# Kernel tuning notes

Hardware: AMD Instinct MI355X
Metric: run time of the kernel (lower is better)

## Reference

```python
import jax, jax.numpy as jnp
import numpy as np

B, S, D = 4, 2048, 1024
H, ADIM = 16, 64
HID = H * ADIM  # 1024


def setup_inputs() -> dict:
    key = jax.random.key(0)
    k1, k2, k3, k4 = jax.random.split(key, 4)
    iQ = jax.random.normal(k1, (B, S, D), dtype=jnp.float32)
    mask = jax.random.randint(k2, (B, S, S), 0, 2).astype(bool)
    Wa = jax.random.normal(k3, (3 * HID, D), dtype=jnp.float32) * (1.0 / np.sqrt(D))
    Wo = jax.random.normal(k4, (HID, HID), dtype=jnp.float32) * (1.0 / np.sqrt(HID))
    return {"iQ": iQ, "mask": mask, "Wa": Wa, "Wo": Wo}


def reference(iQ, mask, Wa, Wo):
    b, s, _ = iQ.shape
    # fused QKV projection: [B,S,3*HID]
    qkv = jnp.einsum("bsd,ed->bse", iQ, Wa)
    q, k, v = jnp.split(qkv, 3, axis=-1)
    # [B,S,HID] -> [B,H,S,ADIM]
    to_heads = lambda t: t.reshape(b, s, H, ADIM).transpose(0, 2, 1, 3)
    q, k, v = to_heads(q), to_heads(k), to_heads(v)
    scores = jnp.einsum("bhqd,bhkd->bhqk", q, k) / np.sqrt(ADIM).astype(np.float32)
    scores = jnp.where(mask[:, None, :, :], jnp.float32(-1e32), scores)
    attn = jax.nn.softmax(scores, axis=-1)
    o = jnp.einsum("bhqk,bhkd->bhqd", attn, v)
    o = o.transpose(0, 2, 1, 3).reshape(b, s, HID)
    return jnp.einsum("bse,oe->bso", o, Wo)
```

## Files before the change

kernel.cpp:

```cpp
#include <hip/hip_runtime.h>
#include <hip/hip_bf16.h>

typedef __bf16 bf16;
typedef __bf16 bfrag __attribute__((ext_vector_type(8)));
typedef float f32x4 __attribute__((ext_vector_type(4)));

constexpr int Bc = 4, Sc = 2048, Hc = 16, ADc = 64, HIDc = 1024;
constexpr size_t QKV_ELEMS = (size_t)Bc * Hc * Sc * ADc;

__device__ __forceinline__ void gload_lds16(const void* g, void* lds) {
  __builtin_amdgcn_global_load_lds(
      (const __attribute__((address_space(1))) unsigned int*)g,
      (__attribute__((address_space(3))) unsigned int*)lds, 16, 0, 0);
}

__device__ __forceinline__ bfrag ldb(const bf16* p) {
  return *(const bfrag*)p;
}

__global__ __launch_bounds__(256) void f2b(const float* __restrict__ s,
                                           bf16* __restrict__ d) {
  const size_t i = ((size_t)blockIdx.x * 256 + threadIdx.x) * 8;
  const float4 a = *(const float4*)(s + i);
  const float4 b = *(const float4*)(s + i + 4);
  bfrag o = {(bf16)a.x, (bf16)a.y, (bf16)a.z, (bf16)a.w,
             (bf16)b.x, (bf16)b.y, (bf16)b.z, (bf16)b.w};
  *(bfrag*)(d + i) = o;
}

template <int MODE>
__global__ __launch_bounds__(256) void gemm_bt(
    const bf16* __restrict__ A,
    const bf16* __restrict__ Bm,
    bf16* __restrict__ C0,
    bf16* __restrict__ C1,
    bf16* __restrict__ C2,
    float* __restrict__ Cf,
    int Kdim, int Ndim)
{
  __shared__ __align__(16) bf16 As[128 * 32];
  __shared__ __align__(16) bf16 Bs[128 * 32];

  const int tid  = threadIdx.x;
  const int wave = tid >> 6;
  const int lane = tid & 63;
  const int n16  = lane & 15;
  const int quad = lane >> 4;
  const int wm   = wave & 1;
  const int wn   = wave >> 1;
  const int m0   = blockIdx.y * 128;
  const int n0   = blockIdx.x * 128;

  const f32x4 fzero = {0.f, 0.f, 0.f, 0.f};
  f32x4 acc[4][4];
#pragma unroll
  for (int i = 0; i < 4; ++i)
#pragma unroll
    for (int j = 0; j < 4; ++j) acc[i][j] = fzero;

  const int lcol = (lane & 3) * 8;

  for (int k0 = 0; k0 < Kdim; k0 += 32) {
#pragma unroll
    for (int c = 0; c < 2; ++c) {
      const int chunk = wave * 2 + c;
      const int row   = chunk * 16 + (lane >> 2);
      const bf16* agp;
      if (MODE == 0) {
        agp = A + (size_t)(m0 + row) * Kdim + k0 + lcol;
      } else {
        const int gs = m0 + row;
        const int h  = k0 >> 6;
        agp = A + (((size_t)(gs >> 11) * Hc + h) * Sc + (gs & 2047)) * ADc
                + (k0 & 63) + lcol;
      }
      gload_lds16(agp, (char*)As + chunk * 1024);
      gload_lds16(Bm + (size_t)(n0 + row) * Kdim + k0 + lcol,
                  (char*)Bs + chunk * 1024);
    }
    __syncthreads();

    bfrag af[4], bf[4];
#pragma unroll
    for (int i = 0; i < 4; ++i)
      af[i] = ldb(As + (wm * 64 + i * 16 + n16) * 32 + quad * 8);
#pragma unroll
    for (int j = 0; j < 4; ++j)
      bf[j] = ldb(Bs + (wn * 64 + j * 16 + n16) * 32 + quad * 8);
#pragma unroll
    for (int i = 0; i < 4; ++i)
#pragma unroll
      for (int j = 0; j < 4; ++j)
        acc[i][j] = __builtin_amdgcn_mfma_f32_16x16x32_bf16(af[i], bf[j], acc[i][j], 0, 0, 0);
    __syncthreads();
  }

#pragma unroll
  for (int i = 0; i < 4; ++i) {
    const int grow = m0 + wm * 64 + i * 16 + quad * 4;
#pragma unroll
    for (int j = 0; j < 4; ++j) {
      const int col_local = wn * 64 + j * 16 + n16;
#pragma unroll
      for (int r = 0; r < 4; ++r) {
        const int row = grow + r;
        const float v = acc[i][j][r];
        if (MODE == 1) {
          Cf[(size_t)row * Ndim + n0 + col_local] = v;
        } else {
          const int seg = n0 >> 10;
          const int hid = (n0 & 1023) + col_local;
          const int h = hid >> 6, a = hid & 63;
          const int bi = row >> 11, s = row & 2047;
          if (seg == 0)
            C0[(((size_t)bi * Hc + h) * Sc + s) * ADc + a] = (bf16)(v * 0.125f);
          else if (seg == 1)
            C1[(((size_t)bi * Hc + h) * Sc + s) * ADc + a] = (bf16)v;
          else
            C2[(((size_t)bi * Hc + h) * ADc + a) * Sc + s] = (bf16)v;
        }
      }
    }
  }
}

__global__ __launch_bounds__(256) void mask_pack(const int* __restrict__ mask,
                                                 unsigned* __restrict__ bits) {
  const int w = blockIdx.x * 256 + threadIdx.x;
  const int4* p = (const int4*)(mask + (size_t)w * 32);
  unsigned out = 0;
#pragma unroll
  for (int i = 0; i < 8; ++i) {
    int4 m = p[i];
    out |= (unsigned)(m.x != 0) << (i * 4);
    out |= (unsigned)(m.y != 0) << (i * 4 + 1);
    out |= (unsigned)(m.z != 0) << (i * 4 + 2);
    out |= (unsigned)(m.w != 0) << (i * 4 + 3);
  }
  bits[w] = out;
}

__global__ __launch_bounds__(512) void attn(
    const bf16* __restrict__ Qw,
    const bf16* __restrict__ Kw,
    const bf16* __restrict__ Vtw,
    const unsigned* __restrict__ mbits,
    bf16* __restrict__ Ow)
{
  __shared__ __align__(16) bf16 Ks[64 * 72];
  __shared__ __align__(16) bf16 Vs[64 * 72];
  __shared__ __align__(16) bf16 Plds[8][16][72];

  const int tid  = threadIdx.x;
  const int wave = tid >> 6, lane = tid & 63;
  const int n16  = lane & 15, quad = lane >> 4;
  const int bh   = blockIdx.x >> 4, qb = blockIdx.x & 15;
  const int b    = bh >> 4;
  const int q0   = qb * 128 + wave * 16;

  const int srow = tid >> 3;
  const int scol = (tid & 7) * 8;
  const bf16* gK = Kw  + ((size_t)bh * Sc + srow) * ADc + scol;
  const bf16* gV = Vtw + ((size_t)bh * ADc + srow) * Sc + scol;
  bf16* lK = Ks + srow * 72 + scol;
  bf16* lV = Vs + srow * 72 + scol;

  const bf16* qrow = Qw + ((size_t)bh * Sc + q0 + n16) * ADc;
  const bfrag qf0 = ldb(qrow + quad * 8);
  const bfrag qf1 = ldb(qrow + 32 + quad * 8);

  const f32x4 fzero = {0.f, 0.f, 0.f, 0.f};
  float li[4] = {0.f, 0.f, 0.f, 0.f};
  f32x4 of[4];
#pragma unroll
  for (int nt = 0; nt < 4; ++nt) of[nt] = fzero;

  const unsigned* mbase = mbits + ((size_t)b * Sc + q0 + quad * 4) * (Sc / 32);

  {
    bfrag k0r = ldb(gK);
    bfrag v0r = ldb(gV);
    *(bfrag*)lK = k0r;
    *(bfrag*)lV = v0r;
  }
  __syncthreads();

  for (int kt = 0; kt < Sc / 64; ++kt) {
    const int kn0 = ((kt + 1) & 31) * 64;
    const bfrag kpre = ldb(gK + (size_t)kn0 * ADc);
    const bfrag vpre = ldb(gV + kn0);

    uint2 mw[4];
#pragma unroll
    for (int r = 0; r < 4; ++r)
      mw[r] = *(const uint2*)(mbase + (size_t)r * (Sc / 32) + kt * 2);

    f32x4 sf[4];
#pragma unroll
    for (int nt = 0; nt < 4; ++nt) {
      const bf16* kr = Ks + (nt * 16 + n16) * 72 + quad * 8;
      const bfrag kf0 = ldb(kr);
      const bfrag kf1 = ldb(kr + 32);
      f32x4 c = fzero;
      c = __builtin_amdgcn_mfma_f32_16x16x32_bf16(qf0, kf0, c, 0, 0, 0);
      c = __builtin_amdgcn_mfma_f32_16x16x32_bf16(qf1, kf1, c, 0, 0, 0);
      sf[nt] = c;
    }

#pragma unroll
    for (int r = 0; r < 4; ++r) {
#pragma unroll
      for (int nt = 0; nt < 4; ++nt) {
        float p = __expf(sf[nt][r]);
        const unsigned word = (nt & 2) ? mw[r].y : mw[r].x;
        if ((word >> ((nt & 1) * 16 + n16)) & 1u) p = 0.f;
        sf[nt][r] = p;
        li[r] += p;
      }
    }

    bf16* pl = &Plds[wave][0][0];
    __asm__ volatile("" ::: "memory");
#pragma unroll
    for (int nt = 0; nt < 4; ++nt)
#pragma unroll
      for (int r = 0; r < 4; ++r)
        pl[(quad * 4 + r) * 72 + nt * 16 + n16] = (bf16)sf[nt][r];
    __asm__ volatile("" ::: "memory");
    const bfrag pf0 = ldb(pl + n16 * 72 + quad * 8);
    const bfrag pf1 = ldb(pl + n16 * 72 + 32 + quad * 8);

#pragma unroll
    for (int nt = 0; nt < 4; ++nt) {
      const bf16* vr = Vs + (nt * 16 + n16) * 72 + quad * 8;
      const bfrag vf0 = ldb(vr);
      const bfrag vf1 = ldb(vr + 32);
      of[nt] = __builtin_amdgcn_mfma_f32_16x16x32_bf16(pf0, vf0, of[nt], 0, 0, 0);
      of[nt] = __builtin_amdgcn_mfma_f32_16x16x32_bf16(pf1, vf1, of[nt], 0, 0, 0);
    }

    __syncthreads();
    *(bfrag*)lK = kpre;
    *(bfrag*)lV = vpre;
    __syncthreads();
  }

#pragma unroll
  for (int r = 0; r < 4; ++r) {
    float s = li[r];
    s += __shfl_xor(s, 1);
    s += __shfl_xor(s, 2);
    s += __shfl_xor(s, 4);
    s += __shfl_xor(s, 8);
    const float inv = 1.f / s;
    const int q = q0 + quad * 4 + r;
    bf16* orow = Ow + ((size_t)bh * Sc + q) * ADc;
#pragma unroll
    for (int nt = 0; nt < 4; ++nt)
      orow[nt * 16 + n16] = (bf16)(of[nt][r] * inv);
  }
}

extern "C" void kernel_launch(void* const* d_in, const int* in_sizes, int n_in,
                              void* d_out, int out_size, void* d_ws, size_t ws_size,
                              hipStream_t stream) {
  const float* iQ = (const float*)d_in[0];
  const int* mask = (const int*)d_in[1];
  const float* Wa = (const float*)d_in[2];
  const float* Wo = (const float*)d_in[3];
  float* out      = (float*)d_out;

  bf16* iQb       = (bf16*)d_out;
  bf16* Wab       = iQb + QKV_ELEMS;
  unsigned* mbits = (unsigned*)(Wab + 3145728);
  bf16* Qw  = (bf16*)d_ws;
  bf16* Kw  = Qw + QKV_ELEMS;
  bf16* Vtw = Kw + QKV_ELEMS;
  bf16* Wob = Vtw + QKV_ELEMS;

  f2b<<<dim3(8388608 / 2048), 256, 0, stream>>>(iQ, iQb);
  f2b<<<dim3(3145728 / 2048), 256, 0, stream>>>(Wa, Wab);
  f2b<<<dim3(1048576 / 2048), 256, 0, stream>>>(Wo, Wob);
  mask_pack<<<dim3((Bc * Sc * Sc / 32) / 256), 256, 0, stream>>>(mask, mbits);
  gemm_bt<0><<<dim3(24, 64), 256, 0, stream>>>(iQb, Wab, Qw, Kw, Vtw, nullptr, 1024, 3072);
  attn<<<dim3(Bc * Hc * 16), 512, 0, stream>>>(Qw, Kw, Vtw, mbits, Qw);
  gemm_bt<1><<<dim3(8, 64), 256, 0, stream>>>(Qw, Wob, nullptr, nullptr, nullptr, out, 1024, 1024);
}
```

Measured before the change: 400.4 us.

## Swizzle K/V LDS tiles and transpose QK^T MFMA for vectorized P stores

Replaces the padded 72-stride K/V shared-memory tiles with unpadded 64-stride tiles that use an XOR swizzle, so fragment reads avoid bank conflicts with less LDS. The QK^T MFMA operands are swapped so each lane holds four consecutive keys for one query row. This lets the mask be read as one word pair per lane, lets P be written to LDS as 4-element vectors instead of scalars, and reduces the row sum to a single accumulator. The final normalization gathers per-row inverses with a shuffle, which adds some cross-lane traffic at the epilogue.

Measured after the change: 376.0 us. 6.1% less time.

```diff
diff --git a/kernel.cpp b/kernel.cpp
--- a/kernel.cpp
+++ b/kernel.cpp
@@ -3,6 +3,7 @@
 
 typedef __bf16 bf16;
 typedef __bf16 bfrag __attribute__((ext_vector_type(8)));
+typedef __bf16 bf16x4 __attribute__((ext_vector_type(4)));
 typedef float f32x4 __attribute__((ext_vector_type(4)));
 
 constexpr int Bc = 4, Sc = 2048, Hc = 16, ADc = 64, HIDc = 1024;
@@ -147,13 +148,14 @@
     const unsigned* __restrict__ mbits,
     bf16* __restrict__ Ow)
 {
-  __shared__ __align__(16) bf16 Ks[64 * 72];
-  __shared__ __align__(16) bf16 Vs[64 * 72];
+  __shared__ __align__(16) bf16 Ks[64 * 64];
+  __shared__ __align__(16) bf16 Vs[64 * 64];
   __shared__ __align__(16) bf16 Plds[8][16][72];
 
   const int tid  = threadIdx.x;
   const int wave = tid >> 6, lane = tid & 63;
   const int n16  = lane & 15, quad = lane >> 4;
+  const int q4   = quad * 4;
   const int bh   = blockIdx.x >> 4, qb = blockIdx.x & 15;
   const int b    = bh >> 4;
   const int q0   = qb * 128 + wave * 16;
@@ -162,20 +164,24 @@
   const int scol = (tid & 7) * 8;
   const bf16* gK = Kw  + ((size_t)bh * Sc + srow) * ADc + scol;
   const bf16* gV = Vtw + ((size_t)bh * ADc + srow) * Sc + scol;
-  bf16* lK = Ks + srow * 72 + scol;
-  bf16* lV = Vs + srow * 72 + scol;
+  bf16* lK = Ks + srow * 64 + (scol ^ ((srow & 7) * 8));
+  bf16* lV = Vs + srow * 64 + (scol ^ ((srow & 7) * 8));
+
+  const int fsw  = (n16 & 7) * 8;
+  const int off0 = (quad * 8) ^ fsw;
+  const int off1 = (32 + quad * 8) ^ fsw;
 
   const bf16* qrow = Qw + ((size_t)bh * Sc + q0 + n16) * ADc;
   const bfrag qf0 = ldb(qrow + quad * 8);
   const bfrag qf1 = ldb(qrow + 32 + quad * 8);
 
   const f32x4 fzero = {0.f, 0.f, 0.f, 0.f};
-  float li[4] = {0.f, 0.f, 0.f, 0.f};
+  float li = 0.f;
   f32x4 of[4];
 #pragma unroll
   for (int nt = 0; nt < 4; ++nt) of[nt] = fzero;
 
-  const unsigned* mbase = mbits + ((size_t)b * Sc + q0 + quad * 4) * (Sc / 32);
+  const unsigned* mq = mbits + ((size_t)b * Sc + q0 + n16) * (Sc / 32);
 
   {
     bfrag k0r = ldb(gK);
@@ -190,51 +196,44 @@
     const bfrag kpre = ldb(gK + (size_t)kn0 * ADc);
     const bfrag vpre = ldb(gV + kn0);
 
-    uint2 mw[4];
-#pragma unroll
-    for (int r = 0; r < 4; ++r)
-      mw[r] = *(const uint2*)(mbase + (size_t)r * (Sc / 32) + kt * 2);
+    const uint2 mwv = *(const uint2*)(mq + kt * 2);
 
     f32x4 sf[4];
 #pragma unroll
     for (int nt = 0; nt < 4; ++nt) {
-      const bf16* kr = Ks + (nt * 16 + n16) * 72 + quad * 8;
-      const bfrag kf0 = ldb(kr);
-      const bfrag kf1 = ldb(kr + 32);
+      const bf16* kr = Ks + (nt * 16 + n16) * 64;
+      const bfrag kf0 = ldb(kr + off0);
+      const bfrag kf1 = ldb(kr + off1);
       f32x4 c = fzero;
-      c = __builtin_amdgcn_mfma_f32_16x16x32_bf16(qf0, kf0, c, 0, 0, 0);
-      c = __builtin_amdgcn_mfma_f32_16x16x32_bf16(qf1, kf1, c, 0, 0, 0);
+      c = __builtin_amdgcn_mfma_f32_16x16x32_bf16(kf0, qf0, c, 0, 0, 0);
+      c = __builtin_amdgcn_mfma_f32_16x16x32_bf16(kf1, qf1, c, 0, 0, 0);
       sf[nt] = c;
-    }
-
-#pragma unroll
-    for (int r = 0; r < 4; ++r) {
-#pragma unroll
-      for (int nt = 0; nt < 4; ++nt) {
-        float p = __expf(sf[nt][r]);
-        const unsigned word = (nt & 2) ? mw[r].y : mw[r].x;
-        if ((word >> ((nt & 1) * 16 + n16)) & 1u) p = 0.f;
-        sf[nt][r] = p;
-        li[r] += p;
-      }
     }
 
     bf16* pl = &Plds[wave][0][0];
     __asm__ volatile("" ::: "memory");
 #pragma unroll
-    for (int nt = 0; nt < 4; ++nt)
-#pragma unroll
-      for (int r = 0; r < 4; ++r)
-        pl[(quad * 4 + r) * 72 + nt * 16 + n16] = (bf16)sf[nt][r];
+    for (int nt = 0; nt < 4; ++nt) {
+      const unsigned word = (nt & 2) ? mwv.y : mwv.x;
+      bf16x4 t;
+#pragma unroll
+      for (int r = 0; r < 4; ++r) {
+        float p = __expf(sf[nt][r]);
+        if ((word >> ((nt & 1) * 16 + q4 + r)) & 1u) p = 0.f;
+        li += p;
+        t[r] = (bf16)p;
+      }
+      *(bf16x4*)(pl + n16 * 72 + nt * 16 + q4) = t;
+    }
     __asm__ volatile("" ::: "memory");
     const bfrag pf0 = ldb(pl + n16 * 72 + quad * 8);
     const bfrag pf1 = ldb(pl + n16 * 72 + 32 + quad * 8);
 
 #pragma unroll
     for (int nt = 0; nt < 4; ++nt) {
-      const bf16* vr = Vs + (nt * 16 + n16) * 72 + quad * 8;
-      const bfrag vf0 = ldb(vr);
-      const bfrag vf1 = ldb(vr + 32);
+      const bf16* vr = Vs + (nt * 16 + n16) * 64;
+      const bfrag vf0 = ldb(vr + off0);
+      const bfrag vf1 = ldb(vr + off1);
       of[nt] = __builtin_amdgcn_mfma_f32_16x16x32_bf16(pf0, vf0, of[nt], 0, 0, 0);
       of[nt] = __builtin_amdgcn_mfma_f32_16x16x32_bf16(pf1, vf1, of[nt], 0, 0, 0);
     }
@@ -245,19 +244,18 @@
     __syncthreads();
   }
 
+  float s = li;
+  s += __shfl_xor(s, 16);
+  s += __shfl_xor(s, 32);
+  const float inv = 1.f / s;
 #pragma unroll
   for (int r = 0; r < 4; ++r) {
-    float s = li[r];
-    s += __shfl_xor(s, 1);
-    s += __shfl_xor(s, 2);
-    s += __shfl_xor(s, 4);
-    s += __shfl_xor(s, 8);
-    const float inv = 1.f / s;
-    const int q = q0 + quad * 4 + r;
+    const float invr = __shfl(inv, q4 + r, 64);
+    const int q = q0 + q4 + r;
     bf16* orow = Ow + ((size_t)bh * Sc + q) * ADc;
 #pragma unroll
     for (int nt = 0; nt < 4; ++nt)
-      orow[nt * 16 + n16] = (bf16)(of[nt][r] * inv);
+      orow[nt * 16 + n16] = (bf16)(of[nt][r] * invr);
   }
 }
 
```
